# Performance work log

Measured on AMD Instinct MI355X. Metric: run time of the kernel, lower is better.

Reference implementation:

```python
import jax, jax.numpy as jnp
import numpy as np

INF = 100000.0


def setup_inputs() -> dict:
    key = jax.random.key(0)
    k1, k2, k3 = jax.random.split(key, 3)
    B, W, T, S, D = 64, 32, 256, 128, 64
    query = jax.random.normal(k1, (S, D), dtype=jnp.float32)
    keys = jax.random.normal(k2, (B, W, T, D), dtype=jnp.float32)
    values = jax.random.normal(k3, (B, W, T, D), dtype=jnp.float32)
    return {"query": query, "keys": keys, "values": values}


def reference(query, keys, values):
    # p: [B, W, S, T] = broadcasted query @ keys^T
    p = jnp.einsum("sd,bwtd->bwst", query, keys)
    # zero scores are masked out with -INF before softmax
    mask = jnp.where(p == 0, -INF, 0.0).astype(p.dtype)
    attn = jax.nn.softmax(p + mask, axis=-1)
    # outputs: [B, W, S, Dv]
    return jnp.einsum("bwst,bwtv->bwsv", attn, values)
```

## Files before the change

kernel.cpp:

```cpp
#include <hip/hip_runtime.h>

typedef _Float16 h16;
typedef __attribute__((ext_vector_type(4))) _Float16 half4v;
typedef __attribute__((ext_vector_type(8))) _Float16 half8v;
typedef __attribute__((ext_vector_type(4))) float f32x4;

static constexpr int Tn = 256;
static constexpr int Dn = 64;
static constexpr int Sn = 128;
static constexpr int KSTR = 72;
static constexpr int PSTR = 40;
static constexpr int VCH  = 64 * KSTR;

#define MFMA_F16 __builtin_amdgcn_mfma_f32_16x16x32_f16

__global__ __launch_bounds__(512, 6)
void attn_kernel(const float* __restrict__ Q, const float* __restrict__ K,
                 const float* __restrict__ V, float* __restrict__ O)
{
    __shared__ __align__(16) h16 KV[Tn * KSTR];
    __shared__ __align__(16) h16 Pb[8 * 16 * PSTR];

    const int head = blockIdx.x;
    const int tid  = threadIdx.x;
    const int wave = tid >> 6;
    const int lane = tid & 63;
    const int quad = lane >> 4;
    const int l16  = lane & 15;

    const float* __restrict__ Kh = K + (size_t)head * (Tn * Dn);
    const float* __restrict__ Vh = V + (size_t)head * (Tn * Dn);
    float* __restrict__ Oh       = O + (size_t)head * (Sn * Dn);

    half8v qf[2];
    {
        const float* qrow = Q + (wave * 16 + l16) * Dn;
#pragma unroll
        for (int kt = 0; kt < 2; ++kt) {
            float4 a = *reinterpret_cast<const float4*>(qrow + kt * 32 + quad * 8);
            float4 b = *reinterpret_cast<const float4*>(qrow + kt * 32 + quad * 8 + 4);
            half8v f;
            f[0] = (h16)a.x; f[1] = (h16)a.y; f[2] = (h16)a.z; f[3] = (h16)a.w;
            f[4] = (h16)b.x; f[5] = (h16)b.y; f[6] = (h16)b.z; f[7] = (h16)b.w;
            qf[kt] = f;
        }
    }

#pragma unroll
    for (int it = 0; it < 8; ++it) {
        int f   = it * 512 + tid;
        int row = f >> 4;
        int c4  = (f & 15) << 2;
        float4 kv = *reinterpret_cast<const float4*>(Kh + row * Dn + c4);
        half4v hv;
        hv[0] = (h16)kv.x; hv[1] = (h16)kv.y; hv[2] = (h16)kv.z; hv[3] = (h16)kv.w;
        *reinterpret_cast<half4v*>(&KV[row * KSTR + c4]) = hv;
    }
    __syncthreads();

    f32x4 acc[16] = {};
#pragma unroll
    for (int n = 0; n < 16; ++n) {
#pragma unroll
        for (int kt = 0; kt < 2; ++kt) {
            half8v bf = *reinterpret_cast<const half8v*>(
                &KV[(n * 16 + l16) * KSTR + kt * 32 + quad * 8]);
            acc[n] = MFMA_F16(qf[kt], bf, acc[n], 0, 0, 0);
        }
    }

    float rinv[4];
#pragma unroll
    for (int r = 0; r < 4; ++r) {
        float mx = -3.0e38f;
#pragma unroll
        for (int n = 0; n < 16; ++n) {
            float p = acc[n][r];
            p = (p == 0.0f) ? -100000.0f : p;
            acc[n][r] = p;
            mx = fmaxf(mx, p);
        }
        mx = fmaxf(mx, __shfl_xor(mx, 1));
        mx = fmaxf(mx, __shfl_xor(mx, 2));
        mx = fmaxf(mx, __shfl_xor(mx, 4));
        mx = fmaxf(mx, __shfl_xor(mx, 8));
        float sm = 0.0f;
#pragma unroll
        for (int n = 0; n < 16; ++n) {
            float e = __expf(acc[n][r] - mx);
            acc[n][r] = e;
            sm += e;
        }
        sm += __shfl_xor(sm, 1);
        sm += __shfl_xor(sm, 2);
        sm += __shfl_xor(sm, 4);
        sm += __shfl_xor(sm, 8);
        rinv[r] = 1.0f / sm;
    }

    __syncthreads();
#pragma unroll
    for (int i = 0; i < 8; ++i) {
        int dbase = (i >> 1) * 16 + quad * 4;
        int t     = ((i & 1) * 8 + wave) * 16 + l16;
        float4 vv = *reinterpret_cast<const float4*>(Vh + t * Dn + dbase);
        int c  = t >> 6;
        int tc = (t & 63) ^ (quad << 3);
        KV[c * VCH + (dbase + 0) * KSTR + tc] = (h16)vv.x;
        KV[c * VCH + (dbase + 1) * KSTR + tc] = (h16)vv.y;
        KV[c * VCH + (dbase + 2) * KSTR + tc] = (h16)vv.z;
        KV[c * VCH + (dbase + 3) * KSTR + tc] = (h16)vv.w;
    }
    __syncthreads();

    f32x4 oacc[4] = {};
    h16* buf = &Pb[wave * 16 * PSTR];
#pragma unroll
    for (int c = 0; c < 8; ++c) {
#pragma unroll
        for (int nn = 0; nn < 2; ++nn) {
            int n = 2 * c + nn;
#pragma unroll
            for (int r = 0; r < 4; ++r) {
                int row = quad * 4 + r;
                int col = (nn * 16 + l16) ^ (quad << 3);
                buf[row * PSTR + col] = (h16)acc[n][r];
            }
        }
        asm volatile("s_waitcnt lgkmcnt(0)" ::: "memory");
        half8v pa = *reinterpret_cast<const half8v*>(
            &buf[l16 * PSTR + ((quad ^ (l16 >> 2)) << 3)]);
#pragma unroll
        for (int dt = 0; dt < 4; ++dt) {
            half8v vb = *reinterpret_cast<const half8v*>(
                &KV[(c >> 1) * VCH + (dt * 16 + l16) * KSTR + (c & 1) * 32 +
                    ((quad ^ (l16 >> 2)) << 3)]);
            oacc[dt] = MFMA_F16(pa, vb, oacc[dt], 0, 0, 0);
        }
    }

#pragma unroll
    for (int dt = 0; dt < 4; ++dt)
#pragma unroll
        for (int r = 0; r < 4; ++r) {
            int s = wave * 16 + quad * 4 + r;
            Oh[s * Dn + dt * 16 + l16] = oacc[dt][r] * rinv[r];
        }
}

extern "C" void kernel_launch(void* const* d_in, const int* in_sizes, int n_in,
                              void* d_out, int out_size, void* d_ws, size_t ws_size,
                              hipStream_t stream) {
    (void)n_in; (void)out_size; (void)d_ws; (void)ws_size;
    const float* q = (const float*)d_in[0];
    const float* k = (const float*)d_in[1];
    const float* v = (const float*)d_in[2];
    float* o = (float*)d_out;
    const int heads = in_sizes[1] / (Tn * Dn);
    attn_kernel<<<dim3(heads), dim3(512), 0, stream>>>(q, k, v, o);
}
```

Baseline: 327.9 us.

## Make attention kernel persistent with double-buffered K prefetch and split V staging

```diff
diff --git a/kernel.cpp b/kernel.cpp
--- a/kernel.cpp
+++ b/kernel.cpp
@@ -14,23 +14,18 @@
 
 #define MFMA_F16 __builtin_amdgcn_mfma_f32_16x16x32_f16
 
-__global__ __launch_bounds__(512, 6)
+__global__ __launch_bounds__(512, 2)
 void attn_kernel(const float* __restrict__ Q, const float* __restrict__ K,
-                 const float* __restrict__ V, float* __restrict__ O)
+                 const float* __restrict__ V, float* __restrict__ O, int nheads)
 {
-    __shared__ __align__(16) h16 KV[Tn * KSTR];
+    __shared__ __align__(16) h16 KV[2][Tn * KSTR];
     __shared__ __align__(16) h16 Pb[8 * 16 * PSTR];
 
-    const int head = blockIdx.x;
     const int tid  = threadIdx.x;
     const int wave = tid >> 6;
     const int lane = tid & 63;
     const int quad = lane >> 4;
     const int l16  = lane & 15;
-
-    const float* __restrict__ Kh = K + (size_t)head * (Tn * Dn);
-    const float* __restrict__ Vh = V + (size_t)head * (Tn * Dn);
-    float* __restrict__ Oh       = O + (size_t)head * (Sn * Dn);
 
     half8v qf[2];
     {
@@ -46,106 +41,195 @@
         }
     }
 
-#pragma unroll
-    for (int it = 0; it < 8; ++it) {
-        int f   = it * 512 + tid;
-        int row = f >> 4;
-        int c4  = (f & 15) << 2;
-        float4 kv = *reinterpret_cast<const float4*>(Kh + row * Dn + c4);
-        half4v hv;
-        hv[0] = (h16)kv.x; hv[1] = (h16)kv.y; hv[2] = (h16)kv.z; hv[3] = (h16)kv.w;
-        *reinterpret_cast<half4v*>(&KV[row * KSTR + c4]) = hv;
+    if ((int)blockIdx.x < nheads) {
+        const float* Kh = K + (size_t)blockIdx.x * (Tn * Dn);
+#pragma unroll
+        for (int it = 0; it < 8; ++it) {
+            int f   = it * 512 + tid;
+            int row = f >> 4;
+            int c4  = (f & 15) << 2;
+            float4 kv = *reinterpret_cast<const float4*>(Kh + row * Dn + c4);
+            half4v hv;
+            hv[0] = (h16)kv.x; hv[1] = (h16)kv.y; hv[2] = (h16)kv.z; hv[3] = (h16)kv.w;
+            *reinterpret_cast<half4v*>(&KV[0][row * KSTR + c4]) = hv;
+        }
     }
     __syncthreads();
 
-    f32x4 acc[16] = {};
-#pragma unroll
-    for (int n = 0; n < 16; ++n) {
-#pragma unroll
-        for (int kt = 0; kt < 2; ++kt) {
-            half8v bf = *reinterpret_cast<const half8v*>(
-                &KV[(n * 16 + l16) * KSTR + kt * 32 + quad * 8]);
-            acc[n] = MFMA_F16(qf[kt], bf, acc[n], 0, 0, 0);
-        }
-    }
-
-    float rinv[4];
-#pragma unroll
-    for (int r = 0; r < 4; ++r) {
-        float mx = -3.0e38f;
-#pragma unroll
-        for (int n = 0; n < 16; ++n) {
-            float p = acc[n][r];
-            p = (p == 0.0f) ? -100000.0f : p;
-            acc[n][r] = p;
-            mx = fmaxf(mx, p);
-        }
-        mx = fmaxf(mx, __shfl_xor(mx, 1));
-        mx = fmaxf(mx, __shfl_xor(mx, 2));
-        mx = fmaxf(mx, __shfl_xor(mx, 4));
-        mx = fmaxf(mx, __shfl_xor(mx, 8));
-        float sm = 0.0f;
-#pragma unroll
-        for (int n = 0; n < 16; ++n) {
-            float e = __expf(acc[n][r] - mx);
-            acc[n][r] = e;
-            sm += e;
-        }
-        sm += __shfl_xor(sm, 1);
-        sm += __shfl_xor(sm, 2);
-        sm += __shfl_xor(sm, 4);
-        sm += __shfl_xor(sm, 8);
-        rinv[r] = 1.0f / sm;
-    }
-
-    __syncthreads();
-#pragma unroll
-    for (int i = 0; i < 8; ++i) {
-        int dbase = (i >> 1) * 16 + quad * 4;
-        int t     = ((i & 1) * 8 + wave) * 16 + l16;
-        float4 vv = *reinterpret_cast<const float4*>(Vh + t * Dn + dbase);
-        int c  = t >> 6;
-        int tc = (t & 63) ^ (quad << 3);
-        KV[c * VCH + (dbase + 0) * KSTR + tc] = (h16)vv.x;
-        KV[c * VCH + (dbase + 1) * KSTR + tc] = (h16)vv.y;
-        KV[c * VCH + (dbase + 2) * KSTR + tc] = (h16)vv.z;
-        KV[c * VCH + (dbase + 3) * KSTR + tc] = (h16)vv.w;
-    }
-    __syncthreads();
-
-    f32x4 oacc[4] = {};
-    h16* buf = &Pb[wave * 16 * PSTR];
-#pragma unroll
-    for (int c = 0; c < 8; ++c) {
-#pragma unroll
-        for (int nn = 0; nn < 2; ++nn) {
-            int n = 2 * c + nn;
+    int cur = 0;
+    for (int head = blockIdx.x; head < nheads; head += gridDim.x) {
+        const float* __restrict__ Vh = V + (size_t)head * (Tn * Dn);
+        float* __restrict__ Oh       = O + (size_t)head * (Sn * Dn);
+        h16* KB = KV[cur];
+
+        f32x4 acc[16] = {};
+        float4 vreg[4];
+
+#pragma unroll
+        for (int j = 0; j < 4; ++j)
+            vreg[j] = *reinterpret_cast<const float4*>(
+                Vh + (wave * 16 + l16) * Dn + j * 16 + quad * 4);
+
+#pragma unroll
+        for (int n = 0; n < 8; ++n)
+#pragma unroll
+            for (int kt = 0; kt < 2; ++kt) {
+                half8v bf = *reinterpret_cast<const half8v*>(
+                    &KB[(n * 16 + l16) * KSTR + kt * 32 + quad * 8]);
+                acc[n] = MFMA_F16(qf[kt], bf, acc[n], 0, 0, 0);
+            }
+        __syncthreads();
+
+#pragma unroll
+        for (int j = 0; j < 4; ++j) {
+            int dbase = j * 16 + quad * 4;
+            int t     = wave * 16 + l16;
+            int c64   = t >> 6;
+            int tc    = (t & 63) ^ (quad << 3);
+            float4 vv = vreg[j];
+            KB[c64 * VCH + (dbase + 0) * KSTR + tc] = (h16)vv.x;
+            KB[c64 * VCH + (dbase + 1) * KSTR + tc] = (h16)vv.y;
+            KB[c64 * VCH + (dbase + 2) * KSTR + tc] = (h16)vv.z;
+            KB[c64 * VCH + (dbase + 3) * KSTR + tc] = (h16)vv.w;
+        }
+
+#pragma unroll
+        for (int j = 0; j < 4; ++j)
+            vreg[j] = *reinterpret_cast<const float4*>(
+                Vh + (128 + wave * 16 + l16) * Dn + j * 16 + quad * 4);
+
+#pragma unroll
+        for (int n = 8; n < 16; ++n)
+#pragma unroll
+            for (int kt = 0; kt < 2; ++kt) {
+                half8v bf = *reinterpret_cast<const half8v*>(
+                    &KB[(n * 16 + l16) * KSTR + kt * 32 + quad * 8]);
+                acc[n] = MFMA_F16(qf[kt], bf, acc[n], 0, 0, 0);
+            }
+        __syncthreads();
+
+#pragma unroll
+        for (int j = 0; j < 4; ++j) {
+            int dbase = j * 16 + quad * 4;
+            int t     = 128 + wave * 16 + l16;
+            int c64   = t >> 6;
+            int tc    = (t & 63) ^ (quad << 3);
+            float4 vv = vreg[j];
+            KB[c64 * VCH + (dbase + 0) * KSTR + tc] = (h16)vv.x;
+            KB[c64 * VCH + (dbase + 1) * KSTR + tc] = (h16)vv.y;
+            KB[c64 * VCH + (dbase + 2) * KSTR + tc] = (h16)vv.z;
+            KB[c64 * VCH + (dbase + 3) * KSTR + tc] = (h16)vv.w;
+        }
+
+        float rinv[4];
+#pragma unroll
+        for (int r = 0; r < 4; ++r) {
+            float mx = -3.0e38f;
+#pragma unroll
+            for (int n = 0; n < 16; ++n) {
+                float p = acc[n][r];
+                p = (p == 0.0f) ? -100000.0f : p;
+                acc[n][r] = p;
+                mx = fmaxf(mx, p);
+            }
+            mx = fmaxf(mx, __shfl_xor(mx, 1));
+            mx = fmaxf(mx, __shfl_xor(mx, 2));
+            mx = fmaxf(mx, __shfl_xor(mx, 4));
+            mx = fmaxf(mx, __shfl_xor(mx, 8));
+            float sm = 0.0f;
+#pragma unroll
+            for (int n = 0; n < 16; ++n) {
+                float e = __expf(acc[n][r] - mx);
+                acc[n][r] = e;
+                sm += e;
+            }
+            sm += __shfl_xor(sm, 1);
+            sm += __shfl_xor(sm, 2);
+            sm += __shfl_xor(sm, 4);
+            sm += __shfl_xor(sm, 8);
+            rinv[r] = 1.0f / sm;
+        }
+        __syncthreads();
+
+        const int  hn = head + gridDim.x;
+        const bool pf = hn < nheads;
+        const float* __restrict__ Kn = K + (size_t)hn * (Tn * Dn);
+        h16* KBn = KV[cur ^ 1];
+        float4 kreg[4];
+        if (pf) {
+#pragma unroll
+            for (int it = 0; it < 4; ++it) {
+                int f = it * 512 + tid;
+                kreg[it] = *reinterpret_cast<const float4*>(Kn + (f >> 4) * Dn + ((f & 15) << 2));
+            }
+        }
+
+        f32x4 oacc[4] = {};
+        h16* buf = &Pb[wave * 16 * PSTR];
+#pragma unroll
+        for (int c = 0; c < 8; ++c) {
+#pragma unroll
+            for (int nn = 0; nn < 2; ++nn) {
+                int n = 2 * c + nn;
+#pragma unroll
+                for (int r = 0; r < 4; ++r) {
+                    int row = quad * 4 + r;
+                    int col = (nn * 16 + l16) ^ (quad << 3);
+                    buf[row * PSTR + col] = (h16)acc[n][r];
+                }
+            }
+            asm volatile("s_waitcnt lgkmcnt(0)" ::: "memory");
+            half8v pa = *reinterpret_cast<const half8v*>(
+                &buf[l16 * PSTR + ((quad ^ (l16 >> 2)) << 3)]);
+#pragma unroll
+            for (int dt = 0; dt < 4; ++dt) {
+                half8v vb = *reinterpret_cast<const half8v*>(
+                    &KB[(c >> 1) * VCH + (dt * 16 + l16) * KSTR + (c & 1) * 32 +
+                        ((quad ^ (l16 >> 2)) << 3)]);
+                oacc[dt] = MFMA_F16(pa, vb, oacc[dt], 0, 0, 0);
+            }
+            if (c == 3 && pf) {
+#pragma unroll
+                for (int it = 0; it < 4; ++it) {
+                    int f   = it * 512 + tid;
+                    int row = f >> 4;
+                    int c4  = (f & 15) << 2;
+                    float4 kv = kreg[it];
+                    half4v hv;
+                    hv[0] = (h16)kv.x; hv[1] = (h16)kv.y; hv[2] = (h16)kv.z; hv[3] = (h16)kv.w;
+                    *reinterpret_cast<half4v*>(&KBn[row * KSTR + c4]) = hv;
+                }
+#pragma unroll
+                for (int it = 0; it < 4; ++it) {
+                    int f = 2048 + it * 512 + tid;
+                    kreg[it] = *reinterpret_cast<const float4*>(Kn + (f >> 4) * Dn + ((f & 15) << 2));
+                }
+            }
+        }
+        if (pf) {
+#pragma unroll
+            for (int it = 0; it < 4; ++it) {
+                int f   = 2048 + it * 512 + tid;
+                int row = f >> 4;
+                int c4  = (f & 15) << 2;
+                float4 kv = kreg[it];
+                half4v hv;
+                hv[0] = (h16)kv.x; hv[1] = (h16)kv.y; hv[2] = (h16)kv.z; hv[3] = (h16)kv.w;
+                *reinterpret_cast<half4v*>(&KBn[row * KSTR + c4]) = hv;
+            }
+        }
+
+#pragma unroll
+        for (int dt = 0; dt < 4; ++dt)
 #pragma unroll
             for (int r = 0; r < 4; ++r) {
-                int row = quad * 4 + r;
-                int col = (nn * 16 + l16) ^ (quad << 3);
-                buf[row * PSTR + col] = (h16)acc[n][r];
-            }
-        }
-        asm volatile("s_waitcnt lgkmcnt(0)" ::: "memory");
-        half8v pa = *reinterpret_cast<const half8v*>(
-            &buf[l16 * PSTR + ((quad ^ (l16 >> 2)) << 3)]);
-#pragma unroll
-        for (int dt = 0; dt < 4; ++dt) {
-            half8v vb = *reinterpret_cast<const half8v*>(
-                &KV[(c >> 1) * VCH + (dt * 16 + l16) * KSTR + (c & 1) * 32 +
-                    ((quad ^ (l16 >> 2)) << 3)]);
-            oacc[dt] = MFMA_F16(pa, vb, oacc[dt], 0, 0, 0);
-        }
-    }
-
-#pragma unroll
-    for (int dt = 0; dt < 4; ++dt)
-#pragma unroll
-        for (int r = 0; r < 4; ++r) {
-            int s = wave * 16 + quad * 4 + r;
-            Oh[s * Dn + dt * 16 + l16] = oacc[dt][r] * rinv[r];
-        }
+                int s = wave * 16 + quad * 4 + r;
+                Oh[s * Dn + dt * 16 + l16] = oacc[dt][r] * rinv[r];
+            }
+
+        __syncthreads();
+        cur ^= 1;
+    }
 }
 
 extern "C" void kernel_launch(void* const* d_in, const int* in_sizes, int n_in,
@@ -157,5 +241,13 @@
     const float* v = (const float*)d_in[2];
     float* o = (float*)d_out;
     const int heads = in_sizes[1] / (Tn * Dn);
-    attn_kernel<<<dim3(heads), dim3(512), 0, stream>>>(q, k, v, o);
+
+    static int ncu = 0;
+    if (ncu == 0) {
+        hipDeviceProp_t prop;
+        ncu = (hipGetDeviceProperties(&prop, 0) == hipSuccess && prop.multiProcessorCount > 0)
+                  ? prop.multiProcessorCount : 256;
+    }
+    int grid = heads < ncu ? heads : ncu;
+    attn_kernel<<<dim3(grid), dim3(512), 0, stream>>>(q, k, v, o, heads);
 }
```

New measurement: 303.5 us. -7.4%, faster.
